# Optimization experiments

Hardware: AMD Instinct MI355X
Metric: run time of the kernel (lower is better)

## Reference

```python
import jax, jax.numpy as jnp
import numpy as np
import math

B, T, D_MODEL, N_HEAD = 2, 2048, 1024, 16
NUM_BUCKETS, MAX_DIST = 32, 128
D_HEAD = D_MODEL // N_HEAD


def _relative_position_bucket(rel_pos, num_buckets=NUM_BUCKETS, max_distance=MAX_DIST):
    # bidirectional=True branch of the torch code
    nb = num_buckets // 2
    buckets = (rel_pos > 0).astype(jnp.int32) * nb
    rel_pos = jnp.abs(rel_pos)
    max_exact = nb // 2
    is_small = rel_pos < max_exact
    # guard log(0); masked out by is_small anyway
    large = max_exact + (
        jnp.log(jnp.maximum(rel_pos, 1).astype(jnp.float32) / max_exact)
        / math.log(max_distance / max_exact) * (nb - max_exact)
    ).astype(jnp.int32)
    large = jnp.minimum(large, nb - 1)
    return buckets + jnp.where(is_small, rel_pos, large)


def compute_bias(rel_bias, q_len, kv_len):
    qp = jnp.arange(q_len, dtype=jnp.int32)[:, None]
    kp = jnp.arange(kv_len, dtype=jnp.int32)[None, :]
    buckets = _relative_position_bucket(kp - qp)          # [Tq, Tkv]
    vals = rel_bias[buckets]                              # [Tq, Tkv, H]
    return jnp.transpose(vals, (2, 0, 1))                 # [H, Tq, Tkv]


def setup_inputs() -> dict:
    key = jax.random.key(0)
    ks = jax.random.split(key, 9)
    inp = {
        'q': jax.random.normal(ks[0], (B, T, D_MODEL), jnp.float32),
        'k': jax.random.normal(ks[1], (B, T, D_MODEL), jnp.float32),
        'v': jax.random.normal(ks[2], (B, T, D_MODEL), jnp.float32),
        'mask': jax.random.randint(ks[3], (B, T, T), 0, 2, jnp.int32),
        'Wq': jax.random.normal(ks[4], (D_MODEL, D_MODEL), jnp.float32) * 0.02,
        'Wk': jax.random.normal(ks[5], (D_MODEL, D_MODEL), jnp.float32) * 0.02,
        'Wv': jax.random.normal(ks[6], (D_MODEL, D_MODEL), jnp.float32) * 0.02,
        'Wfc': jax.random.normal(ks[7], (D_MODEL, D_MODEL), jnp.float32) * 0.02,
        'rel_bias': jax.random.normal(ks[8], (NUM_BUCKETS, N_HEAD), jnp.float32) * 0.02,
    }
    return inp


def reference(q, k, v, mask, Wq, Wk, Wv, Wfc, rel_bias):
    b, tq, _ = q.shape
    tkv = k.shape[1]
    qh = (q @ Wq).reshape(b, tq, N_HEAD, D_HEAD)
    kh = (k @ Wk).reshape(b, tkv, N_HEAD, D_HEAD)
    vh = (v @ Wv).reshape(b, tkv, N_HEAD, D_HEAD)
    attn = jnp.einsum('blhd,bthd->bhlt', qh, kh) / np.sqrt(D_HEAD).astype(np.float32)
    position_bias = compute_bias(rel_bias, tq, tkv)       # [H, Tq, Tkv]
    attn = attn + position_bias[None]                     # broadcast over batch
    attn = jnp.where(mask[:, None] == 0, -1e9, attn)
    attn = jax.nn.softmax(attn, axis=-1)                  # dropout: eval mode (identity)
    out = jnp.einsum('bhlt,bthd->blhd', attn, vh).reshape(b, tq, D_MODEL)
    out = out @ Wfc
    return out, position_bias[:, None]                    # bias returned as [H,1,Tq,Tkv] like torch
```

## Files before the change

kernel.cpp:

```cpp
#include <hip/hip_runtime.h>
#include <math.h>

#define TT 2048
#define BB 2
#define HH 16
#define DMODEL 1024
#define NREL 4095

typedef __attribute__((ext_vector_type(8)))  _Float16 half8;
typedef __attribute__((ext_vector_type(4)))  _Float16 half4;
typedef __attribute__((ext_vector_type(16))) float    f32x16;
typedef __attribute__((ext_vector_type(4)))  int      int4v;

__device__ __forceinline__ f32x16 zero16() {
    f32x16 v;
#pragma unroll
    for (int i = 0; i < 16; ++i) v[i] = 0.f;
    return v;
}

__device__ __forceinline__ unsigned pkh(float a, float b) {
    union { _Float16 h[2]; unsigned u; } x;
    x.h[0] = (_Float16)a; x.h[1] = (_Float16)b;
    return x.u;
}

__device__ __forceinline__ int rel_bucket(int rel) {
    int base = rel > 0 ? 16 : 0;
    int r = rel < 0 ? -rel : rel;
    int lb;
    if (r < 8)       lb = r;
    else if (r < 12) lb = 8;
    else if (r < 16) lb = 9;
    else if (r < 23) lb = 10;
    else if (r < 32) lb = 11;
    else if (r < 46) lb = 12;
    else if (r < 64) lb = 13;
    else if (r < 91) lb = 14;
    else             lb = 15;
    return base + lb;
}

__global__ void bias_table_kernel(const float* __restrict__ rel_bias,
                                  float* __restrict__ btable) {
    int idx = blockIdx.x * blockDim.x + threadIdx.x;
    if (idx >= HH * NREL) return;
    int h = idx / NREL, ri = idx % NREL;
    int bucket = rel_bucket(ri - (TT - 1));
    btable[idx] = rel_bias[bucket * HH + h];
}

__global__ void bias_write_kernel(const float* __restrict__ btable,
                                  float* __restrict__ out1) {
    int n4 = HH * TT * TT / 4;
    int stride = gridDim.x * blockDim.x;
    for (int i4 = blockIdx.x * blockDim.x + threadIdx.x; i4 < n4; i4 += stride) {
        int i = i4 * 4;
        int k = i & (TT - 1);
        int q = (i >> 11) & (TT - 1);
        int h = i >> 22;
        const float* bt = btable + h * NREL + (k - q + (TT - 1));
        float4 v = make_float4(bt[0], bt[1], bt[2], bt[3]);
        reinterpret_cast<float4*>(out1)[i4] = v;
    }
}

__global__ void maskpack_kernel(const int* __restrict__ mask,
                                unsigned* __restrict__ mb) {
    int g = blockIdx.x * 256 + threadIdx.x;
    int v = mask[g];
    unsigned long long bal = __ballot(v != 0);
    if ((g & 63) == 0) {
        int word = g >> 5;
        mb[word]     = (unsigned)bal;
        mb[word + 1] = (unsigned)(bal >> 32);
    }
}

__global__ void cvt16_kernel(const float* __restrict__ in, _Float16* __restrict__ out) {
    int i = blockIdx.x * 256 + threadIdx.x;
    const float4* in4 = (const float4*)in;
    float4 v0 = in4[(size_t)i * 2], v1 = in4[(size_t)i * 2 + 1];
    half8 h = {(_Float16)v0.x, (_Float16)v0.y, (_Float16)v0.z, (_Float16)v0.w,
               (_Float16)v1.x, (_Float16)v1.y, (_Float16)v1.z, (_Float16)v1.w};
    *(half8*)(out + (size_t)i * 8) = h;
}

__global__ __launch_bounds__(256) void wtrans_kernel(const float* __restrict__ W0,
                                                     const float* __restrict__ W1,
                                                     const float* __restrict__ W2,
                                                     const float* __restrict__ W3,
                                                     _Float16* __restrict__ out) {
    int z = blockIdx.z;
    const float* src = z == 0 ? W0 : z == 1 ? W1 : z == 2 ? W2 : W3;
    _Float16* dst = out + (size_t)z * DMODEL * DMODEL;
    __shared__ float t[64][65];
    int k0 = blockIdx.x * 64, n0 = blockIdx.y * 64;
    int tid = threadIdx.x;
    int r = tid >> 4, c4 = (tid & 15) * 4;
#pragma unroll
    for (int i = 0; i < 4; ++i) {
        float4 v = *(const float4*)(src + (size_t)(k0 + r + 16 * i) * DMODEL + n0 + c4);
        t[r + 16 * i][c4] = v.x; t[r + 16 * i][c4 + 1] = v.y;
        t[r + 16 * i][c4 + 2] = v.z; t[r + 16 * i][c4 + 3] = v.w;
    }
    __syncthreads();
    int rn = tid >> 2, ck = (tid & 3) * 16;
    half8 h0, h1;
#pragma unroll
    for (int j = 0; j < 8; ++j) h0[j] = (_Float16)t[ck + j][rn];
#pragma unroll
    for (int j = 0; j < 8; ++j) h1[j] = (_Float16)t[ck + 8 + j][rn];
    *(half8*)(dst + (size_t)(n0 + rn) * DMODEL + k0 + ck) = h0;
    *(half8*)(dst + (size_t)(n0 + rn) * DMODEL + k0 + ck + 8) = h1;
}

__global__ __launch_bounds__(256, 3) void gemm_proj3(
    const _Float16* __restrict__ q16, const _Float16* __restrict__ k16,
    const _Float16* __restrict__ v16, const _Float16* __restrict__ WT,
    _Float16* __restrict__ qhf, _Float16* __restrict__ khf,
    _Float16* __restrict__ vtf, int zbase)
{
    __shared__ char lds[32768];
    int z = zbase + blockIdx.z;
    const _Float16* A  = z == 0 ? q16 : z == 1 ? k16 : v16;
    const _Float16* Bt = WT + (size_t)z * DMODEL * DMODEL;
    int bm = blockIdx.x * 128, bn = blockIdx.y * 128;
    int tid = threadIdx.x;
    int wv = tid >> 6, lane = tid & 63, lo = lane & 31, hi = lane >> 5;
    int wr = wv >> 1, wc = wv & 1;
    int r0 = tid >> 3, s = tid & 7;

    const _Float16* ap[4]; const _Float16* bp[4];
    int awo[4], bwo[4];
#pragma unroll
    for (int c = 0; c < 4; ++c) {
        int r = r0 + 32 * c;
        ap[c] = A  + (size_t)(bm + r) * DMODEL + s * 8;
        bp[c] = Bt + (size_t)(bn + r) * DMODEL + s * 8;
        awo[c] = r * 128 + ((s ^ (r & 7)) << 4);
        bwo[c] = 16384 + r * 128 + ((s ^ (r & 7)) << 4);
    }

    f32x16 acc[2][2];
    acc[0][0] = zero16(); acc[0][1] = zero16();
    acc[1][0] = zero16(); acc[1][1] = zero16();

    half8 pa[4], pb[4];
#pragma unroll
    for (int c = 0; c < 4; ++c) { pa[c] = *(const half8*)ap[c]; pb[c] = *(const half8*)bp[c]; }

    for (int kt = 0; kt < 16; ++kt) {
        __syncthreads();
#pragma unroll
        for (int c = 0; c < 4; ++c) {
            *(half8*)(lds + awo[c]) = pa[c];
            *(half8*)(lds + bwo[c]) = pb[c];
        }
        __syncthreads();
        if (kt < 15) {
#pragma unroll
            for (int c = 0; c < 4; ++c) {
                pa[c] = *(const half8*)(ap[c] + (kt + 1) * 64);
                pb[c] = *(const half8*)(bp[c] + (kt + 1) * 64);
            }
        }
#pragma unroll
        for (int k = 0; k < 4; ++k) {
            int cs = 2 * k + hi;
            half8 a[2], b[2];
#pragma unroll
            for (int i = 0; i < 2; ++i) {
                int ra = wr * 64 + i * 32 + lo;
                a[i] = *(const half8*)(lds + ra * 128 + ((cs ^ (ra & 7)) << 4));
                int rb = wc * 64 + i * 32 + lo;
                b[i] = *(const half8*)(lds + 16384 + rb * 128 + ((cs ^ (rb & 7)) << 4));
            }
            acc[0][0] = __builtin_amdgcn_mfma_f32_32x32x16_f16(a[0], b[0], acc[0][0], 0, 0, 0);
            acc[0][1] = __builtin_amdgcn_mfma_f32_32x32x16_f16(a[0], b[1], acc[0][1], 0, 0, 0);
            acc[1][0] = __builtin_amdgcn_mfma_f32_32x32x16_f16(a[1], b[0], acc[1][0], 0, 0, 0);
            acc[1][1] = __builtin_amdgcn_mfma_f32_32x32x16_f16(a[1], b[1], acc[1][1], 0, 0, 0);
        }
    }

    if (z < 2) {
        _Float16* C = z == 0 ? qhf : khf;
#pragma unroll
        for (int j = 0; j < 2; ++j) {
            int n = bn + wc * 64 + j * 32 + lo;
            int h = n >> 6, d = n & 63;
#pragma unroll
            for (int i = 0; i < 2; ++i) {
                int mb = bm + wr * 64 + i * 32 + 4 * hi;
#pragma unroll
                for (int r = 0; r < 16; ++r) {
                    int m = mb + (r & 3) + 8 * (r >> 2);
                    int b = m >> 11, t = m & (TT - 1);
                    C[((size_t)(b * HH + h) * TT + t) * 64 + d] = (_Float16)acc[i][j][r];
                }
            }
        }
    } else {
#pragma unroll
        for (int j = 0; j < 2; ++j) {
            int n = bn + wc * 64 + j * 32 + lo;
            int h = n >> 6, d = n & 63;
#pragma unroll
            for (int i = 0; i < 2; ++i) {
                int mb = bm + wr * 64 + i * 32 + 4 * hi;
                int b = mb >> 11, tb = mb & (TT - 1);
#pragma unroll
                for (int r4 = 0; r4 < 4; ++r4) {
                    half4 hv = {(_Float16)acc[i][j][4 * r4 + 0], (_Float16)acc[i][j][4 * r4 + 1],
                                (_Float16)acc[i][j][4 * r4 + 2], (_Float16)acc[i][j][4 * r4 + 3]};
                    *(half4*)(vtf + ((size_t)(b * HH + h) * 64 + d) * TT + tb + 8 * r4) = hv;
                }
            }
        }
    }
}

__global__ __launch_bounds__(256, 3) void gemm_fc(
    const _Float16* __restrict__ O, const _Float16* __restrict__ Bt,
    float* __restrict__ out0)
{
    __shared__ char lds[32768];
    int bm = blockIdx.x * 128, bn = blockIdx.y * 128;
    int tid = threadIdx.x;
    int wv = tid >> 6, lane = tid & 63, lo = lane & 31, hi = lane >> 5;
    int wr = wv >> 1, wc = wv & 1;
    int r0 = tid >> 3, s = tid & 7;
    int bb = bm >> 11, tbase = bm & (TT - 1);

    const _Float16* ap[4]; const _Float16* bp[4];
    int awo[4], bwo[4];
#pragma unroll
    for (int c = 0; c < 4; ++c) {
        int r = r0 + 32 * c;
        ap[c] = O  + ((size_t)(bb * HH) * TT + tbase + r) * 64 + s * 8;
        bp[c] = Bt + (size_t)(bn + r) * DMODEL + s * 8;
        awo[c] = r * 128 + ((s ^ (r & 7)) << 4);
        bwo[c] = 16384 + r * 128 + ((s ^ (r & 7)) << 4);
    }

    f32x16 acc[2][2];
    acc[0][0] = zero16(); acc[0][1] = zero16();
    acc[1][0] = zero16(); acc[1][1] = zero16();

    half8 pa[4], pb[4];
#pragma unroll
    for (int c = 0; c < 4; ++c) { pa[c] = *(const half8*)ap[c]; pb[c] = *(const half8*)bp[c]; }

    for (int kt = 0; kt < 16; ++kt) {
        __syncthreads();
#pragma unroll
        for (int c = 0; c < 4; ++c) {
            *(half8*)(lds + awo[c]) = pa[c];
            *(half8*)(lds + bwo[c]) = pb[c];
        }
        __syncthreads();
        if (kt < 15) {
#pragma unroll
            for (int c = 0; c < 4; ++c) {
                pa[c] = *(const half8*)(ap[c] + (size_t)(kt + 1) * TT * 64);
                pb[c] = *(const half8*)(bp[c] + (kt + 1) * 64);
            }
        }
#pragma unroll
        for (int k = 0; k < 4; ++k) {
            int cs = 2 * k + hi;
            half8 a[2], b[2];
#pragma unroll
            for (int i = 0; i < 2; ++i) {
                int ra = wr * 64 + i * 32 + lo;
                a[i] = *(const half8*)(lds + ra * 128 + ((cs ^ (ra & 7)) << 4));
                int rb = wc * 64 + i * 32 + lo;
                b[i] = *(const half8*)(lds + 16384 + rb * 128 + ((cs ^ (rb & 7)) << 4));
            }
            acc[0][0] = __builtin_amdgcn_mfma_f32_32x32x16_f16(a[0], b[0], acc[0][0], 0, 0, 0);
            acc[0][1] = __builtin_amdgcn_mfma_f32_32x32x16_f16(a[0], b[1], acc[0][1], 0, 0, 0);
            acc[1][0] = __builtin_amdgcn_mfma_f32_32x32x16_f16(a[1], b[0], acc[1][0], 0, 0, 0);
            acc[1][1] = __builtin_amdgcn_mfma_f32_32x32x16_f16(a[1], b[1], acc[1][1], 0, 0, 0);
        }
    }

#pragma unroll
    for (int j = 0; j < 2; ++j) {
        int n = bn + wc * 64 + j * 32 + lo;
#pragma unroll
        for (int i = 0; i < 2; ++i) {
            int mb = bm + wr * 64 + i * 32 + 4 * hi;
#pragma unroll
            for (int r = 0; r < 16; ++r) {
                int m = mb + (r & 3) + 8 * (r >> 2);
                out0[(size_t)m * DMODEL + n] = acc[i][j][r];
            }
        }
    }
}

__global__ __launch_bounds__(256) void attn_mfma(
    const _Float16* __restrict__ qh, const _Float16* __restrict__ kh,
    const _Float16* __restrict__ vt, const unsigned* __restrict__ maskbits,
    const float* __restrict__ btable, _Float16* __restrict__ Oout)
{
    int bid = blockIdx.x;
    int xcd = bid & 7, j = bid >> 3;
    int qt = j & 15, bh = xcd + 8 * (j >> 4);
    int h = bh & 15, b = bh >> 4;
    int tid = threadIdx.x;
    int wv = tid >> 6, lane = tid & 63, lo = lane & 31, hi = lane >> 5;
    int q0 = qt * 128 + wv * 32;

    const size_t bhoff = (size_t)(b * HH + h);
    const _Float16* Q = qh + (bhoff * TT + q0) * 64;
    const _Float16* K = kh + bhoff * TT * 64;
    const _Float16* V = vt + bhoff * 64 * TT;

    half8 qf[4];
#pragma unroll
    for (int c = 0; c < 4; ++c)
        qf[c] = *(const half8*)(Q + (size_t)lo * 64 + c * 16 + hi * 8);

    const float* bt = btable + h * NREL + (TT - 1) - (q0 + lo) + 4 * hi;
    const unsigned* mw = maskbits + ((size_t)b * TT + q0 + lo) * 64;

    f32x16 acco0 = zero16(), acco1 = zero16();
    float m = -INFINITY, l = 0.f;

    for (int kt = 0; kt < TT / 64; ++kt) {
        int k0 = kt * 64;
        half8 kf[2][4], vf[2][4];
#pragma unroll
        for (int g = 0; g < 2; ++g)
#pragma unroll
            for (int c = 0; c < 4; ++c)
                kf[g][c] = *(const half8*)(K + (size_t)(k0 + 32 * g + lo) * 64 + c * 16 + hi * 8);
        unsigned wm0 = mw[2 * kt], wm1 = mw[2 * kt + 1];
#pragma unroll
        for (int dg = 0; dg < 2; ++dg)
#pragma unroll
            for (int c = 0; c < 4; ++c)
                vf[dg][c] = *(const half8*)(V + (size_t)(32 * dg + lo) * TT + k0 + c * 16 + hi * 8);
        float bias[2][16];
#pragma unroll
        for (int g = 0; g < 2; ++g)
#pragma unroll
            for (int r = 0; r < 16; ++r)
                bias[g][r] = bt[k0 + (r & 3) + 8 * (r >> 2) + 32 * g];

        f32x16 accs0 = zero16(), accs1 = zero16();
#pragma unroll
        for (int c = 0; c < 4; ++c) {
            accs0 = __builtin_amdgcn_mfma_f32_32x32x16_f16(kf[0][c], qf[c], accs0, 0, 0, 0);
            accs1 = __builtin_amdgcn_mfma_f32_32x32x16_f16(kf[1][c], qf[c], accs1, 0, 0, 0);
        }

        float p[2][16];
        unsigned ws0 = wm0 >> (hi * 4), ws1 = wm1 >> (hi * 4);
#pragma unroll
        for (int r = 0; r < 16; ++r) {
            int sh = (r & 3) + 8 * (r >> 2);
            float s0 = fmaf(accs0[r], 0.125f, bias[0][r]);
            float s1 = fmaf(accs1[r], 0.125f, bias[1][r]);
            p[0][r] = ((ws0 >> sh) & 1) ? s0 : -1e9f;
            p[1][r] = ((ws1 >> sh) & 1) ? s1 : -1e9f;
        }

        float tm = p[0][0];
#pragma unroll
        for (int g = 0; g < 2; ++g)
#pragma unroll
            for (int r = 0; r < 16; ++r) tm = fmaxf(tm, p[g][r]);
        tm = fmaxf(tm, __shfl_xor(tm, 32));
        float mnew = fmaxf(m, tm);
        float corr = __expf(m - mnew);
        float rs = 0.f;
#pragma unroll
        for (int g = 0; g < 2; ++g)
#pragma unroll
            for (int r = 0; r < 16; ++r) {
                p[g][r] = __expf(p[g][r] - mnew);
                rs += p[g][r];
            }
        rs += __shfl_xor(rs, 32);
        l = l * corr + rs; m = mnew;
#pragma unroll
        for (int r = 0; r < 16; ++r) { acco0[r] *= corr; acco1[r] *= corr; }

        half8 pb[4];
#pragma unroll
        for (int g = 0; g < 2; ++g)
#pragma unroll
            for (int hc = 0; hc < 2; ++hc) {
                int r0 = hc * 8;
                unsigned w0 = pkh(p[g][r0 + 0], p[g][r0 + 1]);
                unsigned w2 = pkh(p[g][r0 + 4], p[g][r0 + 5]);
                asm("v_permlane32_swap_b32 %0, %1" : "+v"(w0), "+v"(w2));
                unsigned w1 = pkh(p[g][r0 + 2], p[g][r0 + 3]);
                unsigned w3 = pkh(p[g][r0 + 6], p[g][r0 + 7]);
                asm("v_permlane32_swap_b32 %0, %1" : "+v"(w1), "+v"(w3));
                union { int4v i; half8 hf; } cv;
                cv.i = (int4v){(int)w0, (int)w1, (int)w2, (int)w3};
                pb[2 * g + hc] = cv.hf;
            }

#pragma unroll
        for (int c = 0; c < 4; ++c) {
            acco0 = __builtin_amdgcn_mfma_f32_32x32x16_f16(vf[0][c], pb[c], acco0, 0, 0, 0);
            acco1 = __builtin_amdgcn_mfma_f32_32x32x16_f16(vf[1][c], pb[c], acco1, 0, 0, 0);
        }
    }

    float inv = 1.f / l;
    _Float16* op = Oout + (bhoff * TT + q0 + lo) * 64;
#pragma unroll
    for (int r4 = 0; r4 < 4; ++r4) {
        int d0 = 8 * r4 + 4 * hi;
        half4 h0 = {(_Float16)(acco0[4 * r4 + 0] * inv), (_Float16)(acco0[4 * r4 + 1] * inv),
                    (_Float16)(acco0[4 * r4 + 2] * inv), (_Float16)(acco0[4 * r4 + 3] * inv)};
        *(half4*)(op + d0) = h0;
        half4 h1 = {(_Float16)(acco1[4 * r4 + 0] * inv), (_Float16)(acco1[4 * r4 + 1] * inv),
                    (_Float16)(acco1[4 * r4 + 2] * inv), (_Float16)(acco1[4 * r4 + 3] * inv)};
        *(half4*)(op + d0 + 32) = h1;
    }
}

extern "C" void kernel_launch(void* const* d_in, const int* in_sizes, int n_in,
                              void* d_out, int out_size, void* d_ws, size_t ws_size,
                              hipStream_t stream) {
    const float* q        = (const float*)d_in[0];
    const float* k        = (const float*)d_in[1];
    const float* v        = (const float*)d_in[2];
    const int*   mask     = (const int*)  d_in[3];
    const float* Wq       = (const float*)d_in[4];
    const float* Wk       = (const float*)d_in[5];
    const float* Wv       = (const float*)d_in[6];
    const float* Wfc      = (const float*)d_in[7];
    const float* rel_bias = (const float*)d_in[8];

    float* out0 = (float*)d_out;
    float* out1 = out0 + (size_t)BB * TT * DMODEL;

    char* w = (char*)d_ws;
    _Float16* q16 = (_Float16*)(w);
    _Float16* k16 = (_Float16*)(w + ((size_t)8  << 20));
    _Float16* v16 = (_Float16*)(w + ((size_t)16 << 20));
    _Float16* qhf = (_Float16*)(w + ((size_t)24 << 20));
    _Float16* khf = (_Float16*)(w + ((size_t)32 << 20));
    _Float16* WT  = (_Float16*)(w + ((size_t)40 << 20));
    float*    btable = (float*)(w + ((size_t)48 << 20));
    unsigned* mbits  = (unsigned*)(w + ((size_t)48 << 20) + ((size_t)1 << 19));
    bool big = ws_size >= ((size_t)58 << 20);
    _Float16* vtf = big ? (_Float16*)(w + ((size_t)49 << 20) + ((size_t)1 << 19))
                        : k16;
    _Float16* O = q16;

    bias_table_kernel<<<dim3((HH * NREL + 255) / 256), dim3(256), 0, stream>>>(rel_bias, btable);
    maskpack_kernel<<<dim3(BB * TT * TT / 256), dim3(256), 0, stream>>>(mask, mbits);

    cvt16_kernel<<<dim3(2048), dim3(256), 0, stream>>>(q, q16);
    cvt16_kernel<<<dim3(2048), dim3(256), 0, stream>>>(k, k16);
    cvt16_kernel<<<dim3(2048), dim3(256), 0, stream>>>(v, v16);
    wtrans_kernel<<<dim3(16, 16, 4), dim3(256), 0, stream>>>(Wq, Wk, Wv, Wfc, WT);

    if (big) {
        gemm_proj3<<<dim3(32, 8, 3), dim3(256), 0, stream>>>(q16, k16, v16, WT,
                                                             qhf, khf, vtf, 0);
    } else {
        gemm_proj3<<<dim3(32, 8, 1), dim3(256), 0, stream>>>(q16, k16, v16, WT, qhf, khf, vtf, 0);
        gemm_proj3<<<dim3(32, 8, 1), dim3(256), 0, stream>>>(q16, k16, v16, WT, qhf, khf, vtf, 1);
        gemm_proj3<<<dim3(32, 8, 1), dim3(256), 0, stream>>>(q16, k16, v16, WT, qhf, khf, vtf, 2);
    }

    bias_write_kernel<<<dim3(2048), dim3(256), 0, stream>>>(btable, out1);

    attn_mfma<<<dim3(BB * HH * 16), dim3(256), 0, stream>>>(
        qhf, khf, vtf, mbits, btable, O);

    gemm_fc<<<dim3(32, 8), dim3(256), 0, stream>>>(O, WT + (size_t)3 * DMODEL * DMODEL, out0);
}
```

Measured before the change: 302.8 us.

## Merge prep kernels, use direct global-to-LDS loads, fuse bias write with FC GEMM

Six preprocessing kernels are merged into one prep_kernel that dispatches on block index, cutting launch overhead. The projection and FC GEMMs now use global_load_lds to copy tiles straight into LDS, replacing the register-staged prefetch and the XOR swizzle, and gemm_proj3 raises its occupancy bound. The bias-matrix write is moved into the FC GEMM launch as extra blocks so both run concurrently. Attention defers the V loads, reads bias directly instead of holding it in registers, and raises wave priority around the MFMA sections. In exchange, the GEMM loses its register double-buffering and its LDS swizzle, which may add LDS bank conflicts and expose load latency.

```diff
diff --git a/kernel.cpp b/kernel.cpp
--- a/kernel.cpp
+++ b/kernel.cpp
@@ -23,6 +23,12 @@
     union { _Float16 h[2]; unsigned u; } x;
     x.h[0] = (_Float16)a; x.h[1] = (_Float16)b;
     return x.u;
+}
+
+__device__ __forceinline__ void gload16(const void* g, void* l) {
+    __builtin_amdgcn_global_load_lds(
+        (const __attribute__((address_space(1))) void*)g,
+        (__attribute__((address_space(3))) void*)l, 16, 0, 0);
 }
 
 __device__ __forceinline__ int rel_bucket(int rel) {
@@ -41,87 +47,74 @@
     return base + lb;
 }
 
-__global__ void bias_table_kernel(const float* __restrict__ rel_bias,
-                                  float* __restrict__ btable) {
-    int idx = blockIdx.x * blockDim.x + threadIdx.x;
-    if (idx >= HH * NREL) return;
-    int h = idx / NREL, ri = idx % NREL;
-    int bucket = rel_bucket(ri - (TT - 1));
-    btable[idx] = rel_bias[bucket * HH + h];
-}
-
-__global__ void bias_write_kernel(const float* __restrict__ btable,
-                                  float* __restrict__ out1) {
-    int n4 = HH * TT * TT / 4;
-    int stride = gridDim.x * blockDim.x;
-    for (int i4 = blockIdx.x * blockDim.x + threadIdx.x; i4 < n4; i4 += stride) {
-        int i = i4 * 4;
-        int k = i & (TT - 1);
-        int q = (i >> 11) & (TT - 1);
-        int h = i >> 22;
-        const float* bt = btable + h * NREL + (k - q + (TT - 1));
-        float4 v = make_float4(bt[0], bt[1], bt[2], bt[3]);
-        reinterpret_cast<float4*>(out1)[i4] = v;
-    }
-}
-
-__global__ void maskpack_kernel(const int* __restrict__ mask,
-                                unsigned* __restrict__ mb) {
-    int g = blockIdx.x * 256 + threadIdx.x;
-    int v = mask[g];
-    unsigned long long bal = __ballot(v != 0);
-    if ((g & 63) == 0) {
-        int word = g >> 5;
-        mb[word]     = (unsigned)bal;
-        mb[word + 1] = (unsigned)(bal >> 32);
-    }
-}
-
-__global__ void cvt16_kernel(const float* __restrict__ in, _Float16* __restrict__ out) {
-    int i = blockIdx.x * 256 + threadIdx.x;
-    const float4* in4 = (const float4*)in;
-    float4 v0 = in4[(size_t)i * 2], v1 = in4[(size_t)i * 2 + 1];
-    half8 h = {(_Float16)v0.x, (_Float16)v0.y, (_Float16)v0.z, (_Float16)v0.w,
-               (_Float16)v1.x, (_Float16)v1.y, (_Float16)v1.z, (_Float16)v1.w};
-    *(half8*)(out + (size_t)i * 8) = h;
-}
-
-__global__ __launch_bounds__(256) void wtrans_kernel(const float* __restrict__ W0,
-                                                     const float* __restrict__ W1,
-                                                     const float* __restrict__ W2,
-                                                     const float* __restrict__ W3,
-                                                     _Float16* __restrict__ out) {
-    int z = blockIdx.z;
-    const float* src = z == 0 ? W0 : z == 1 ? W1 : z == 2 ? W2 : W3;
-    _Float16* dst = out + (size_t)z * DMODEL * DMODEL;
+__global__ __launch_bounds__(256) void prep_kernel(
+    const float* __restrict__ q, const float* __restrict__ k,
+    const float* __restrict__ v, const int* __restrict__ mask,
+    const float* __restrict__ W0, const float* __restrict__ W1,
+    const float* __restrict__ W2, const float* __restrict__ W3,
+    const float* __restrict__ rel_bias,
+    _Float16* __restrict__ q16, _Float16* __restrict__ k16,
+    _Float16* __restrict__ v16, _Float16* __restrict__ WT,
+    float* __restrict__ btable, unsigned* __restrict__ mb)
+{
     __shared__ float t[64][65];
-    int k0 = blockIdx.x * 64, n0 = blockIdx.y * 64;
-    int tid = threadIdx.x;
-    int r = tid >> 4, c4 = (tid & 15) * 4;
-#pragma unroll
-    for (int i = 0; i < 4; ++i) {
-        float4 v = *(const float4*)(src + (size_t)(k0 + r + 16 * i) * DMODEL + n0 + c4);
-        t[r + 16 * i][c4] = v.x; t[r + 16 * i][c4 + 1] = v.y;
-        t[r + 16 * i][c4 + 2] = v.z; t[r + 16 * i][c4 + 3] = v.w;
-    }
-    __syncthreads();
-    int rn = tid >> 2, ck = (tid & 3) * 16;
-    half8 h0, h1;
-#pragma unroll
-    for (int j = 0; j < 8; ++j) h0[j] = (_Float16)t[ck + j][rn];
-#pragma unroll
-    for (int j = 0; j < 8; ++j) h1[j] = (_Float16)t[ck + 8 + j][rn];
-    *(half8*)(dst + (size_t)(n0 + rn) * DMODEL + k0 + ck) = h0;
-    *(half8*)(dst + (size_t)(n0 + rn) * DMODEL + k0 + ck + 8) = h1;
-}
-
-__global__ __launch_bounds__(256, 3) void gemm_proj3(
+    int bid = blockIdx.x, tid = threadIdx.x;
+    if (bid < 256) {
+        int idx = bid * 256 + tid;
+        if (idx < HH * NREL) {
+            int h = idx / NREL, ri = idx % NREL;
+            btable[idx] = rel_bias[rel_bucket(ri - (TT - 1)) * HH + h];
+        }
+    } else if (bid < 1280) {
+        int zz = (bid - 256) >> 8, inner = (bid - 256) & 255;
+        const float* src = zz == 0 ? W0 : zz == 1 ? W1 : zz == 2 ? W2 : W3;
+        _Float16* dst = WT + (size_t)zz * DMODEL * DMODEL;
+        int k0 = (inner >> 4) * 64, n0 = (inner & 15) * 64;
+        int r = tid >> 4, c4 = (tid & 15) * 4;
+#pragma unroll
+        for (int i = 0; i < 4; ++i) {
+            float4 vv = *(const float4*)(src + (size_t)(k0 + r + 16 * i) * DMODEL + n0 + c4);
+            t[r + 16 * i][c4] = vv.x; t[r + 16 * i][c4 + 1] = vv.y;
+            t[r + 16 * i][c4 + 2] = vv.z; t[r + 16 * i][c4 + 3] = vv.w;
+        }
+        __syncthreads();
+        int rn = tid >> 2, ck = (tid & 3) * 16;
+        half8 h0, h1;
+#pragma unroll
+        for (int j = 0; j < 8; ++j) h0[j] = (_Float16)t[ck + j][rn];
+#pragma unroll
+        for (int j = 0; j < 8; ++j) h1[j] = (_Float16)t[ck + 8 + j][rn];
+        *(half8*)(dst + (size_t)(n0 + rn) * DMODEL + k0 + ck) = h0;
+        *(half8*)(dst + (size_t)(n0 + rn) * DMODEL + k0 + ck + 8) = h1;
+    } else if (bid < 7424) {
+        int zz = (bid - 1280) >> 11, inner = (bid - 1280) & 2047;
+        const float* src = zz == 0 ? q : zz == 1 ? k : v;
+        _Float16* dst = zz == 0 ? q16 : zz == 1 ? k16 : v16;
+        int i = inner * 256 + tid;
+        const float4* in4 = (const float4*)src;
+        float4 v0 = in4[(size_t)i * 2], v1 = in4[(size_t)i * 2 + 1];
+        half8 h = {(_Float16)v0.x, (_Float16)v0.y, (_Float16)v0.z, (_Float16)v0.w,
+                   (_Float16)v1.x, (_Float16)v1.y, (_Float16)v1.z, (_Float16)v1.w};
+        *(half8*)(dst + (size_t)i * 8) = h;
+    } else {
+        int g = (bid - 7424) * 256 + tid;
+        int vv = mask[g];
+        unsigned long long bal = __ballot(vv != 0);
+        if ((g & 63) == 0) {
+            int word = g >> 5;
+            mb[word]     = (unsigned)bal;
+            mb[word + 1] = (unsigned)(bal >> 32);
+        }
+    }
+}
+
+__global__ __launch_bounds__(256, 4) void gemm_proj3(
     const _Float16* __restrict__ q16, const _Float16* __restrict__ k16,
     const _Float16* __restrict__ v16, const _Float16* __restrict__ WT,
     _Float16* __restrict__ qhf, _Float16* __restrict__ khf,
     _Float16* __restrict__ vtf, int zbase)
 {
-    __shared__ char lds[32768];
+    __shared__ __align__(16) char lds[32768];
     int z = zbase + blockIdx.z;
     const _Float16* A  = z == 0 ? q16 : z == 1 ? k16 : v16;
     const _Float16* Bt = WT + (size_t)z * DMODEL * DMODEL;
@@ -129,58 +122,37 @@
     int tid = threadIdx.x;
     int wv = tid >> 6, lane = tid & 63, lo = lane & 31, hi = lane >> 5;
     int wr = wv >> 1, wc = wv & 1;
-    int r0 = tid >> 3, s = tid & 7;
-
-    const _Float16* ap[4]; const _Float16* bp[4];
-    int awo[4], bwo[4];
-#pragma unroll
-    for (int c = 0; c < 4; ++c) {
-        int r = r0 + 32 * c;
-        ap[c] = A  + (size_t)(bm + r) * DMODEL + s * 8;
-        bp[c] = Bt + (size_t)(bn + r) * DMODEL + s * 8;
-        awo[c] = r * 128 + ((s ^ (r & 7)) << 4);
-        bwo[c] = 16384 + r * 128 + ((s ^ (r & 7)) << 4);
-    }
+    int srow = wv * 32 + (lane >> 3);
+    int scol = (lane & 7) * 8;
 
     f32x16 acc[2][2];
     acc[0][0] = zero16(); acc[0][1] = zero16();
     acc[1][0] = zero16(); acc[1][1] = zero16();
 
-    half8 pa[4], pb[4];
-#pragma unroll
-    for (int c = 0; c < 4; ++c) { pa[c] = *(const half8*)ap[c]; pb[c] = *(const half8*)bp[c]; }
-
     for (int kt = 0; kt < 16; ++kt) {
+#pragma unroll
+        for (int t = 0; t < 4; ++t) {
+            gload16(A  + (size_t)(bm + srow + t * 8) * DMODEL + kt * 64 + scol,
+                    lds + wv * 4096 + t * 1024);
+            gload16(Bt + (size_t)(bn + srow + t * 8) * DMODEL + kt * 64 + scol,
+                    lds + 16384 + wv * 4096 + t * 1024);
+        }
         __syncthreads();
 #pragma unroll
-        for (int c = 0; c < 4; ++c) {
-            *(half8*)(lds + awo[c]) = pa[c];
-            *(half8*)(lds + bwo[c]) = pb[c];
-        }
-        __syncthreads();
-        if (kt < 15) {
-#pragma unroll
-            for (int c = 0; c < 4; ++c) {
-                pa[c] = *(const half8*)(ap[c] + (kt + 1) * 64);
-                pb[c] = *(const half8*)(bp[c] + (kt + 1) * 64);
-            }
-        }
-#pragma unroll
-        for (int k = 0; k < 4; ++k) {
-            int cs = 2 * k + hi;
+        for (int kk = 0; kk < 4; ++kk) {
+            int cs = 2 * kk + hi;
             half8 a[2], b[2];
 #pragma unroll
             for (int i = 0; i < 2; ++i) {
-                int ra = wr * 64 + i * 32 + lo;
-                a[i] = *(const half8*)(lds + ra * 128 + ((cs ^ (ra & 7)) << 4));
-                int rb = wc * 64 + i * 32 + lo;
-                b[i] = *(const half8*)(lds + 16384 + rb * 128 + ((cs ^ (rb & 7)) << 4));
+                a[i] = *(const half8*)(lds + (wr * 64 + i * 32 + lo) * 128 + cs * 16);
+                b[i] = *(const half8*)(lds + 16384 + (wc * 64 + i * 32 + lo) * 128 + cs * 16);
             }
             acc[0][0] = __builtin_amdgcn_mfma_f32_32x32x16_f16(a[0], b[0], acc[0][0], 0, 0, 0);
             acc[0][1] = __builtin_amdgcn_mfma_f32_32x32x16_f16(a[0], b[1], acc[0][1], 0, 0, 0);
             acc[1][0] = __builtin_amdgcn_mfma_f32_32x32x16_f16(a[1], b[0], acc[1][0], 0, 0, 0);
             acc[1][1] = __builtin_amdgcn_mfma_f32_32x32x16_f16(a[1], b[1], acc[1][1], 0, 0, 0);
         }
+        __syncthreads();
     }
 
     if (z < 2) {
@@ -191,10 +163,10 @@
             int h = n >> 6, d = n & 63;
 #pragma unroll
             for (int i = 0; i < 2; ++i) {
-                int mb = bm + wr * 64 + i * 32 + 4 * hi;
+                int mb2 = bm + wr * 64 + i * 32 + 4 * hi;
 #pragma unroll
                 for (int r = 0; r < 16; ++r) {
-                    int m = mb + (r & 3) + 8 * (r >> 2);
+                    int m = mb2 + (r & 3) + 8 * (r >> 2);
                     int b = m >> 11, t = m & (TT - 1);
                     C[((size_t)(b * HH + h) * TT + t) * 64 + d] = (_Float16)acc[i][j][r];
                 }
@@ -207,93 +179,14 @@
             int h = n >> 6, d = n & 63;
 #pragma unroll
             for (int i = 0; i < 2; ++i) {
-                int mb = bm + wr * 64 + i * 32 + 4 * hi;
-                int b = mb >> 11, tb = mb & (TT - 1);
+                int mb2 = bm + wr * 64 + i * 32 + 4 * hi;
+                int b = mb2 >> 11, tb = mb2 & (TT - 1);
 #pragma unroll
                 for (int r4 = 0; r4 < 4; ++r4) {
                     half4 hv = {(_Float16)acc[i][j][4 * r4 + 0], (_Float16)acc[i][j][4 * r4 + 1],
                                 (_Float16)acc[i][j][4 * r4 + 2], (_Float16)acc[i][j][4 * r4 + 3]};
                     *(half4*)(vtf + ((size_t)(b * HH + h) * 64 + d) * TT + tb + 8 * r4) = hv;
                 }
-            }
-        }
-    }
-}
-
-__global__ __launch_bounds__(256, 3) void gemm_fc(
-    const _Float16* __restrict__ O, const _Float16* __restrict__ Bt,
-    float* __restrict__ out0)
-{
-    __shared__ char lds[32768];
-    int bm = blockIdx.x * 128, bn = blockIdx.y * 128;
-    int tid = threadIdx.x;
-    int wv = tid >> 6, lane = tid & 63, lo = lane & 31, hi = lane >> 5;
-    int wr = wv >> 1, wc = wv & 1;
-    int r0 = tid >> 3, s = tid & 7;
-    int bb = bm >> 11, tbase = bm & (TT - 1);
-
-    const _Float16* ap[4]; const _Float16* bp[4];
-    int awo[4], bwo[4];
-#pragma unroll
-    for (int c = 0; c < 4; ++c) {
-        int r = r0 + 32 * c;
-        ap[c] = O  + ((size_t)(bb * HH) * TT + tbase + r) * 64 + s * 8;
-        bp[c] = Bt + (size_t)(bn + r) * DMODEL + s * 8;
-        awo[c] = r * 128 + ((s ^ (r & 7)) << 4);
-        bwo[c] = 16384 + r * 128 + ((s ^ (r & 7)) << 4);
-    }
-
-    f32x16 acc[2][2];
-    acc[0][0] = zero16(); acc[0][1] = zero16();
-    acc[1][0] = zero16(); acc[1][1] = zero16();
-
-    half8 pa[4], pb[4];
-#pragma unroll
-    for (int c = 0; c < 4; ++c) { pa[c] = *(const half8*)ap[c]; pb[c] = *(const half8*)bp[c]; }
-
-    for (int kt = 0; kt < 16; ++kt) {
-        __syncthreads();
-#pragma unroll
-        for (int c = 0; c < 4; ++c) {
-            *(half8*)(lds + awo[c]) = pa[c];
-            *(half8*)(lds + bwo[c]) = pb[c];
-        }
-        __syncthreads();
-        if (kt < 15) {
-#pragma unroll
-            for (int c = 0; c < 4; ++c) {
-                pa[c] = *(const half8*)(ap[c] + (size_t)(kt + 1) * TT * 64);
-                pb[c] = *(const half8*)(bp[c] + (kt + 1) * 64);
-            }
-        }
-#pragma unroll
-        for (int k = 0; k < 4; ++k) {
-            int cs = 2 * k + hi;
-            half8 a[2], b[2];
-#pragma unroll
-            for (int i = 0; i < 2; ++i) {
-                int ra = wr * 64 + i * 32 + lo;
-                a[i] = *(const half8*)(lds + ra * 128 + ((cs ^ (ra & 7)) << 4));
-                int rb = wc * 64 + i * 32 + lo;
-                b[i] = *(const half8*)(lds + 16384 + rb * 128 + ((cs ^ (rb & 7)) << 4));
-            }
-            acc[0][0] = __builtin_amdgcn_mfma_f32_32x32x16_f16(a[0], b[0], acc[0][0], 0, 0, 0);
-            acc[0][1] = __builtin_amdgcn_mfma_f32_32x32x16_f16(a[0], b[1], acc[0][1], 0, 0, 0);
-            acc[1][0] = __builtin_amdgcn_mfma_f32_32x32x16_f16(a[1], b[0], acc[1][0], 0, 0, 0);
-            acc[1][1] = __builtin_amdgcn_mfma_f32_32x32x16_f16(a[1], b[1], acc[1][1], 0, 0, 0);
-        }
-    }
-
-#pragma unroll
-    for (int j = 0; j < 2; ++j) {
-        int n = bn + wc * 64 + j * 32 + lo;
-#pragma unroll
-        for (int i = 0; i < 2; ++i) {
-            int mb = bm + wr * 64 + i * 32 + 4 * hi;
-#pragma unroll
-            for (int r = 0; r < 16; ++r) {
-                int m = mb + (r & 3) + 8 * (r >> 2);
-                out0[(size_t)m * DMODEL + n] = acc[i][j][r];
             }
         }
     }
@@ -330,39 +223,30 @@
 
     for (int kt = 0; kt < TT / 64; ++kt) {
         int k0 = kt * 64;
-        half8 kf[2][4], vf[2][4];
+        half8 kf[2][4];
 #pragma unroll
         for (int g = 0; g < 2; ++g)
 #pragma unroll
             for (int c = 0; c < 4; ++c)
                 kf[g][c] = *(const half8*)(K + (size_t)(k0 + 32 * g + lo) * 64 + c * 16 + hi * 8);
         unsigned wm0 = mw[2 * kt], wm1 = mw[2 * kt + 1];
-#pragma unroll
-        for (int dg = 0; dg < 2; ++dg)
-#pragma unroll
-            for (int c = 0; c < 4; ++c)
-                vf[dg][c] = *(const half8*)(V + (size_t)(32 * dg + lo) * TT + k0 + c * 16 + hi * 8);
-        float bias[2][16];
-#pragma unroll
-        for (int g = 0; g < 2; ++g)
-#pragma unroll
-            for (int r = 0; r < 16; ++r)
-                bias[g][r] = bt[k0 + (r & 3) + 8 * (r >> 2) + 32 * g];
 
         f32x16 accs0 = zero16(), accs1 = zero16();
+        __builtin_amdgcn_s_setprio(1);
 #pragma unroll
         for (int c = 0; c < 4; ++c) {
             accs0 = __builtin_amdgcn_mfma_f32_32x32x16_f16(kf[0][c], qf[c], accs0, 0, 0, 0);
             accs1 = __builtin_amdgcn_mfma_f32_32x32x16_f16(kf[1][c], qf[c], accs1, 0, 0, 0);
         }
+        __builtin_amdgcn_s_setprio(0);
 
         float p[2][16];
         unsigned ws0 = wm0 >> (hi * 4), ws1 = wm1 >> (hi * 4);
 #pragma unroll
         for (int r = 0; r < 16; ++r) {
             int sh = (r & 3) + 8 * (r >> 2);
-            float s0 = fmaf(accs0[r], 0.125f, bias[0][r]);
-            float s1 = fmaf(accs1[r], 0.125f, bias[1][r]);
+            float s0 = fmaf(accs0[r], 0.125f, bt[k0 + sh]);
+            float s1 = fmaf(accs1[r], 0.125f, bt[k0 + sh + 32]);
             p[0][r] = ((ws0 >> sh) & 1) ? s0 : -1e9f;
             p[1][r] = ((ws1 >> sh) & 1) ? s1 : -1e9f;
         }
@@ -387,6 +271,13 @@
         l = l * corr + rs; m = mnew;
 #pragma unroll
         for (int r = 0; r < 16; ++r) { acco0[r] *= corr; acco1[r] *= corr; }
+
+        half8 vf[2][4];
+#pragma unroll
+        for (int dg = 0; dg < 2; ++dg)
+#pragma unroll
+            for (int c = 0; c < 4; ++c)
+                vf[dg][c] = *(const half8*)(V + (size_t)(32 * dg + lo) * TT + k0 + c * 16 + hi * 8);
 
         half8 pb[4];
 #pragma unroll
@@ -405,11 +296,13 @@
                 pb[2 * g + hc] = cv.hf;
             }
 
+        __builtin_amdgcn_s_setprio(1);
 #pragma unroll
         for (int c = 0; c < 4; ++c) {
             acco0 = __builtin_amdgcn_mfma_f32_32x32x16_f16(vf[0][c], pb[c], acco0, 0, 0, 0);
             acco1 = __builtin_amdgcn_mfma_f32_32x32x16_f16(vf[1][c], pb[c], acco1, 0, 0, 0);
         }
+        __builtin_amdgcn_s_setprio(0);
     }
 
     float inv = 1.f / l;
@@ -423,6 +316,79 @@
         half4 h1 = {(_Float16)(acco1[4 * r4 + 0] * inv), (_Float16)(acco1[4 * r4 + 1] * inv),
                     (_Float16)(acco1[4 * r4 + 2] * inv), (_Float16)(acco1[4 * r4 + 3] * inv)};
         *(half4*)(op + d0 + 32) = h1;
+    }
+}
+
+__global__ __launch_bounds__(256) void fc_bias_kernel(
+    const _Float16* __restrict__ O, const _Float16* __restrict__ Bt,
+    float* __restrict__ out0, const float* __restrict__ btable,
+    float* __restrict__ out1)
+{
+    __shared__ __align__(16) char lds[32768];
+    int bid = blockIdx.x, tid = threadIdx.x;
+    if (bid >= 256) {
+        const int n4 = HH * TT * TT / 4, stride = 2048 * 256;
+        for (int i4 = (bid - 256) * 256 + tid; i4 < n4; i4 += stride) {
+            int i = i4 * 4;
+            int kk = i & (TT - 1);
+            int qq = (i >> 11) & (TT - 1);
+            int hh2 = i >> 22;
+            const float* btp = btable + hh2 * NREL + (kk - qq + (TT - 1));
+            float4 vv = make_float4(btp[0], btp[1], btp[2], btp[3]);
+            reinterpret_cast<float4*>(out1)[i4] = vv;
+        }
+        return;
+    }
+    int bm = (bid & 31) * 128, bn = (bid >> 5) * 128;
+    int wv = tid >> 6, lane = tid & 63, lo = lane & 31, hi = lane >> 5;
+    int wr = wv >> 1, wc = wv & 1;
+    int srow = wv * 32 + (lane >> 3);
+    int scol = (lane & 7) * 8;
+    int bb = bm >> 11, tbase = bm & (TT - 1);
+
+    f32x16 acc[2][2];
+    acc[0][0] = zero16(); acc[0][1] = zero16();
+    acc[1][0] = zero16(); acc[1][1] = zero16();
+
+    for (int kt = 0; kt < 16; ++kt) {
+        const _Float16* Ab = O + ((size_t)(bb * HH + kt) * TT + tbase) * 64;
+#pragma unroll
+        for (int t = 0; t < 4; ++t) {
+            gload16(Ab + (size_t)(srow + t * 8) * 64 + scol,
+                    lds + wv * 4096 + t * 1024);
+            gload16(Bt + (size_t)(bn + srow + t * 8) * DMODEL + kt * 64 + scol,
+                    lds + 16384 + wv * 4096 + t * 1024);
+        }
+        __syncthreads();
+#pragma unroll
+        for (int kk = 0; kk < 4; ++kk) {
+            int cs = 2 * kk + hi;
+            half8 a[2], b[2];
+#pragma unroll
+            for (int i = 0; i < 2; ++i) {
+                a[i] = *(const half8*)(lds + (wr * 64 + i * 32 + lo) * 128 + cs * 16);
+                b[i] = *(const half8*)(lds + 16384 + (wc * 64 + i * 32 + lo) * 128 + cs * 16);
+            }
+            acc[0][0] = __builtin_amdgcn_mfma_f32_32x32x16_f16(a[0], b[0], acc[0][0], 0, 0, 0);
+            acc[0][1] = __builtin_amdgcn_mfma_f32_32x32x16_f16(a[0], b[1], acc[0][1], 0, 0, 0);
+            acc[1][0] = __builtin_amdgcn_mfma_f32_32x32x16_f16(a[1], b[0], acc[1][0], 0, 0, 0);
+            acc[1][1] = __builtin_amdgcn_mfma_f32_32x32x16_f16(a[1], b[1], acc[1][1], 0, 0, 0);
+        }
+        __syncthreads();
+    }
+
+#pragma unroll
+    for (int j = 0; j < 2; ++j) {
+        int n = bn + wc * 64 + j * 32 + lo;
+#pragma unroll
+        for (int i = 0; i < 2; ++i) {
+            int mb2 = bm + wr * 64 + i * 32 + 4 * hi;
+#pragma unroll
+            for (int r = 0; r < 16; ++r) {
+                int m = mb2 + (r & 3) + 8 * (r >> 2);
+                out0[(size_t)m * DMODEL + n] = acc[i][j][r];
+            }
+        }
     }
 }
 
@@ -456,13 +422,8 @@
                         : k16;
     _Float16* O = q16;
 
-    bias_table_kernel<<<dim3((HH * NREL + 255) / 256), dim3(256), 0, stream>>>(rel_bias, btable);
-    maskpack_kernel<<<dim3(BB * TT * TT / 256), dim3(256), 0, stream>>>(mask, mbits);
-
-    cvt16_kernel<<<dim3(2048), dim3(256), 0, stream>>>(q, q16);
-    cvt16_kernel<<<dim3(2048), dim3(256), 0, stream>>>(k, k16);
-    cvt16_kernel<<<dim3(2048), dim3(256), 0, stream>>>(v, v16);
-    wtrans_kernel<<<dim3(16, 16, 4), dim3(256), 0, stream>>>(Wq, Wk, Wv, Wfc, WT);
+    prep_kernel<<<dim3(40192), dim3(256), 0, stream>>>(
+        q, k, v, mask, Wq, Wk, Wv, Wfc, rel_bias, q16, k16, v16, WT, btable, mbits);
 
     if (big) {
         gemm_proj3<<<dim3(32, 8, 3), dim3(256), 0, stream>>>(q16, k16, v16, WT,
@@ -473,10 +434,9 @@
         gemm_proj3<<<dim3(32, 8, 1), dim3(256), 0, stream>>>(q16, k16, v16, WT, qhf, khf, vtf, 2);
     }
 
-    bias_write_kernel<<<dim3(2048), dim3(256), 0, stream>>>(btable, out1);
-
     attn_mfma<<<dim3(BB * HH * 16), dim3(256), 0, stream>>>(
         qhf, khf, vtf, mbits, btable, O);
 
-    gemm_fc<<<dim3(32, 8), dim3(256), 0, stream>>>(O, WT + (size_t)3 * DMODEL * DMODEL, out0);
-}
+    fc_bias_kernel<<<dim3(2304), dim3(256), 0, stream>>>(
+        O, WT + (size_t)3 * DMODEL * DMODEL, out0, btable, out1);
+}
```

Result: faster. 291.2 us (-3.8%).
